# Optimization experiments

Measured on AMD Instinct MI355X. Metric: run time of the kernel, lower is better.

The kernel has to match this reference:

```python
import jax, jax.numpy as jnp
import numpy as np
import math

H = 16
D_MODEL = 1024
D_K = D_MODEL // H


def setup_inputs() -> dict:
    key = jax.random.key(0)
    ks = jax.random.split(key, 12)
    B, S = 4, 2048
    inp = {
        "query": jax.random.normal(ks[0], (B, S, D_MODEL), jnp.float32),
        "key": jax.random.normal(ks[1], (B, S, D_MODEL), jnp.float32),
        "value": jax.random.normal(ks[2], (B, S, D_MODEL), jnp.float32),
        # causal mask, broadcastable over heads: [B, 1, S, S]
        "mask": jnp.broadcast_to(jnp.tril(jnp.ones((S, S), bool)), (B, 1, S, S)),
    }
    sc = 1.0 / math.sqrt(D_MODEL)
    inp["Wq"] = jax.random.normal(ks[3], (D_MODEL, D_MODEL), jnp.float32) * sc
    inp["bq"] = jnp.zeros((D_MODEL,), jnp.float32)
    inp["Wk"] = jax.random.normal(ks[4], (D_MODEL, D_MODEL), jnp.float32) * sc
    inp["bk"] = jnp.zeros((D_MODEL,), jnp.float32)
    inp["Wv"] = jax.random.normal(ks[5], (D_MODEL, D_MODEL), jnp.float32) * sc
    inp["bv"] = jnp.zeros((D_MODEL,), jnp.float32)
    inp["Wo"] = jax.random.normal(ks[6], (D_MODEL, D_MODEL), jnp.float32) * sc
    inp["bo"] = jnp.zeros((D_MODEL,), jnp.float32)
    return inp


def reference(query, key, value, mask, Wq, bq, Wk, bk, Wv, bv, Wo, bo):
    B, S, D = query.shape
    # torch nn.Linear: y = x @ W.T + b; then view(B,-1,h,d_k).transpose(1,2)
    def proj(x, W, b):
        return (x @ W.T + b).reshape(B, -1, H, D_K).transpose(0, 2, 1, 3)  # [B,h,S,d_k]

    q = proj(query, Wq, bq)
    k = proj(key, Wk, bk)
    v = proj(value, Wv, bv)

    scores = jnp.einsum("bhqd,bhkd->bhqk", q, k) / math.sqrt(D_K)
    scores = jnp.where(mask, scores, jnp.finfo(scores.dtype).min)
    p_attn = jax.nn.softmax(scores, axis=-1)  # dropout: eval mode (identity)
    x = jnp.einsum("bhqk,bhkd->bhqd", p_attn, v)
    x = x.transpose(0, 2, 1, 3).reshape(B, -1, H * D_K)
    return x @ Wo.T + bo
```

## Files before the change

kernel.cpp:

```cpp
#include <hip/hip_runtime.h>
#include <hip/hip_bf16.h>

typedef unsigned short u16;
typedef unsigned int u32;
typedef __attribute__((ext_vector_type(8))) short short8;
typedef __attribute__((ext_vector_type(4))) short short4v;
typedef __attribute__((ext_vector_type(4))) float f32x4;
typedef __attribute__((ext_vector_type(4))) float float4_t;

#define DIM 1024
#define NH  16
#define DKK 64
#define SEQ 2048
#define NB  4
#define HDSZ ((size_t)NB * NH * SEQ * DKK)
#define WSZ  ((size_t)DIM * DIM)
#define SM_SCALE 0.1803368801111244f

__device__ __forceinline__ u16 f2bf(float f) {
    __bf16 h = (__bf16)f;
    return __builtin_bit_cast(u16, h);
}

__device__ __forceinline__ f32x4 mfma_bf16(short8 a, short8 b, f32x4 c) {
    return __builtin_amdgcn_mfma_f32_16x16x32_bf16(a, b, c, 0, 0, 0);
}

__device__ __forceinline__ short8 pack8(float4_t a, float4_t b) {
    short8 v;
    v[0] = (short)f2bf(a[0]); v[1] = (short)f2bf(a[1]);
    v[2] = (short)f2bf(a[2]); v[3] = (short)f2bf(a[3]);
    v[4] = (short)f2bf(b[0]); v[5] = (short)f2bf(b[1]);
    v[6] = (short)f2bf(b[2]); v[7] = (short)f2bf(b[3]);
    return v;
}

typedef const __attribute__((address_space(1))) u32* gas1_t;
typedef __attribute__((address_space(3))) u32* las3_t;
__device__ __forceinline__ void g2l16(const void* g, void* l) {
    __builtin_amdgcn_global_load_lds((gas1_t)g, (las3_t)l, 16, 0, 0);
}

__device__ __forceinline__ float max16(const f32x4* s) {
    const float a = fmaxf(fmaxf(s[0][0], s[0][1]), fmaxf(s[0][2], s[0][3]));
    const float b = fmaxf(fmaxf(s[1][0], s[1][1]), fmaxf(s[1][2], s[1][3]));
    const float c = fmaxf(fmaxf(s[2][0], s[2][1]), fmaxf(s[2][2], s[2][3]));
    const float d = fmaxf(fmaxf(s[3][0], s[3][1]), fmaxf(s[3][2], s[3][3]));
    return fmaxf(fmaxf(a, b), fmaxf(c, d));
}

__global__ __launch_bounds__(256)
void convall(const float* __restrict__ q, const float* __restrict__ k,
             const float* __restrict__ v,
             const float* __restrict__ w0, const float* __restrict__ w1,
             const float* __restrict__ w2, const float* __restrict__ w3,
             u16* __restrict__ dq, u16* __restrict__ dk, u16* __restrict__ dv,
             u16* __restrict__ dw)
{
    const int y = blockIdx.y;
    const float* src;
    u16* dst;
    if (y < 4) {
        src = y == 0 ? w0 : y == 1 ? w1 : y == 2 ? w2 : w3;
        dst = dw + (size_t)y * WSZ;
    } else {
        const int a = (y - 4) >> 3, c = (y - 4) & 7;
        src = (a == 0 ? q : a == 1 ? k : v) + (size_t)c * WSZ;
        dst = (a == 0 ? dq : a == 1 ? dk : dv) + (size_t)c * WSZ;
    }
    const size_t i = ((size_t)blockIdx.x * 256 + threadIdx.x) * 8;
    const float4_t a = *(const float4_t*)(src + i);
    const float4_t b = *(const float4_t*)(src + i + 4);
    *(short8*)(dst + i) = pack8(a, b);
}

template<int MODE>
__global__ __launch_bounds__(256)
void gemmb(const u16* __restrict__ A0, const u16* __restrict__ A1,
           const u16* __restrict__ Wb,
           const float* __restrict__ b0, const float* __restrict__ b1,
           u16* __restrict__ Cb, float* __restrict__ Cf)
{
    __shared__ __align__(16) u16 As[128][64];
    __shared__ __align__(16) u16 Bs[128][64];
    const int tid  = threadIdx.x;
    const int lane = tid & 63;
    const int w    = tid >> 6;
    const int wr   = w >> 1, wc = w & 1;
    const int m0   = blockIdx.y * 128;
    const int n0   = blockIdx.x * 128;
    const int z    = (MODE == 0) ? blockIdx.z : 0;
    const int lm   = lane & 15, lg = lane >> 4;
    const int srow   = lane >> 3;
    const int schunk = (lane & 7) ^ srow;

    const u16* A  = (MODE == 0) ? (z ? A1 : A0) : A0;
    const u16* Bw = (MODE == 2) ? A1 : Wb + (size_t)z * WSZ;

    f32x4 acc[4][4];
#pragma unroll
    for (int i = 0; i < 4; ++i)
#pragma unroll
        for (int j = 0; j < 4; ++j) acc[i][j] = (f32x4){0.f, 0.f, 0.f, 0.f};

    for (int k0 = 0; k0 < DIM; k0 += 64) {
        __syncthreads();
#pragma unroll
        for (int i = 0; i < 4; ++i) {
            g2l16(A  + (size_t)(m0 + w * 32 + i * 8 + srow) * DIM + k0 + schunk * 8,
                  &As[w * 32 + i * 8][0]);
            g2l16(Bw + (size_t)(n0 + w * 32 + i * 8 + srow) * DIM + k0 + schunk * 8,
                  &Bs[w * 32 + i * 8][0]);
        }
        __syncthreads();

        short8 af[2][4], bfr[2][4];
#pragma unroll
        for (int t = 0; t < 4; ++t)
#pragma unroll
            for (int kh = 0; kh < 2; ++kh) {
                const int c = (kh * 4 + lg) ^ (lm & 7);
                af[kh][t]  = *(const short8*)&As[wr * 64 + t * 16 + lm][c * 8];
                bfr[kh][t] = *(const short8*)&Bs[wc * 64 + t * 16 + lm][c * 8];
            }
#pragma unroll
        for (int mt = 0; mt < 4; ++mt)
#pragma unroll
            for (int nt = 0; nt < 4; ++nt) {
                acc[mt][nt] = mfma_bf16(af[0][mt], bfr[0][nt], acc[mt][nt]);
                acc[mt][nt] = mfma_bf16(af[1][mt], bfr[1][nt], acc[mt][nt]);
            }
    }

    const float scale = (MODE == 0 && z == 0) ? SM_SCALE : 1.f;
    const float* bias = (MODE == 0 && z) ? b1 : b0;
    u16* Cz = (MODE == 0) ? Cb + (size_t)z * HDSZ : Cb;

#pragma unroll
    for (int mt = 0; mt < 4; ++mt)
#pragma unroll
        for (int nt = 0; nt < 4; ++nt)
#pragma unroll
            for (int r = 0; r < 4; ++r) {
                const int m = m0 + wr * 64 + mt * 16 + lg * 4 + r;
                const int n = n0 + wc * 64 + nt * 16 + lm;
                if (MODE == 0) {
                    const float val = (acc[mt][nt][r] + bias[n]) * scale;
                    const int b = m >> 11, s = m & 2047;
                    const int h = n >> 6,  dk = n & 63;
                    Cz[(((size_t)b * NH + h) * SEQ + s) * DKK + dk] = f2bf(val);
                } else if (MODE == 1) {
                    Cf[(size_t)m * DIM + n] = acc[mt][nt][r] + bias[n];
                } else {
                    const float val = acc[mt][nt][r] + bias[m];
                    const int h = m >> 6, dk = m & 63;
                    const int b = n >> 11, s = n & 2047;
                    Cz[(((size_t)b * NH + h) * DKK + dk) * SEQ + s] = f2bf(val);
                }
            }
}

__global__ __launch_bounds__(256, 2)
void attn3(const u16* __restrict__ Q, const u16* __restrict__ K,
           const u16* __restrict__ Vt, u16* __restrict__ O)
{
    __shared__ __align__(16) u16 Ks[64][72];
    __shared__ __align__(16) u16 Vs[64][72];
    __shared__ __align__(16) u16 Ps[4][32][72];

    const int tid  = threadIdx.x;
    const int lane = tid & 63;
    const int w    = tid >> 6;
    const int lm   = lane & 15, lg = lane >> 4;
    const int Lr   = blockIdx.y * gridDim.x + blockIdx.x;
    const int work = (Lr & 7) * 128 + (Lr >> 3);
    const int pb   = work & 15;
    const int bh   = work >> 4;
    const int Abase = pb * 64;
    const int Bbase = SEQ - 64 - Abase;
    const int qA = Abase + 16 * w;
    const int qB = Bbase + 16 * w;
    const u16* Qp = Q  + (size_t)bh * SEQ * DKK;
    const u16* Kp = K  + (size_t)bh * SEQ * DKK;
    const u16* Vp = Vt + (size_t)bh * DKK * SEQ;

    short8 qa[2][2];
#pragma unroll
    for (int kh = 0; kh < 2; ++kh) {
        qa[0][kh] = *(const short8*)(Qp + (size_t)(qA + lm) * DKK + kh * 32 + lg * 8);
        qa[1][kh] = *(const short8*)(Qp + (size_t)(qB + lm) * DKK + kh * 32 + lg * 8);
    }

    float m_q[2] = {-INFINITY, -INFINITY};
    float l_q[2] = {0.f, 0.f};
    f32x4 o[2][4];
#pragma unroll
    for (int qt = 0; qt < 2; ++qt)
#pragma unroll
        for (int dt = 0; dt < 4; ++dt) o[qt][dt] = (f32x4){0.f, 0.f, 0.f, 0.f};

    const f32x4 zero = (f32x4){0.f, 0.f, 0.f, 0.f};
    const int srow = tid >> 3;
    const int soct = (tid & 7) * 8;
    const int kv_end = Bbase + 64;

    short8 rk0 = *(const short8*)(Kp + (size_t)srow * DKK + soct);
    short8 rk1 = *(const short8*)(Kp + (size_t)(srow + 32) * DKK + soct);
    short8 rv0 = *(const short8*)(Vp + (size_t)srow * SEQ + soct);
    short8 rv1 = *(const short8*)(Vp + (size_t)(srow + 32) * SEQ + soct);

    for (int kv0 = 0; kv0 < kv_end; kv0 += 64) {
        __syncthreads();
        *(short8*)&Ks[srow][soct]      = rk0;
        *(short8*)&Ks[srow + 32][soct] = rk1;
        *(short8*)&Vs[srow][soct]      = rv0;
        *(short8*)&Vs[srow + 32][soct] = rv1;
        const int nkv = kv0 + 64;
        if (nkv < kv_end) {
            rk0 = *(const short8*)(Kp + (size_t)(nkv + srow) * DKK + soct);
            rk1 = *(const short8*)(Kp + (size_t)(nkv + srow + 32) * DKK + soct);
            rv0 = *(const short8*)(Vp + (size_t)srow * SEQ + nkv + soct);
            rv1 = *(const short8*)(Vp + (size_t)(srow + 32) * SEQ + nkv + soct);
        }
        __syncthreads();

        const bool actA = kv0 < qA + 16;
        const bool msk[2] = { kv0 + 63 > qA, kv0 + 63 > qB };
        const int  qb[2]  = { qA, qB };

        f32x4 s[2][4];
#pragma unroll
        for (int kvt = 0; kvt < 4; ++kvt) {
            const short8 kb0 = *(const short8*)&Ks[kvt * 16 + lm][lg * 8];
            const short8 kb1 = *(const short8*)&Ks[kvt * 16 + lm][32 + lg * 8];
            s[1][kvt] = mfma_bf16(kb1, qa[1][1], mfma_bf16(kb0, qa[1][0], zero));
            if (actA)
                s[0][kvt] = mfma_bf16(kb1, qa[0][1], mfma_bf16(kb0, qa[0][0], zero));
        }

        float mx[2] = {-INFINITY, -INFINITY};
#pragma unroll
        for (int qt = 0; qt < 2; ++qt) {
            if (!qt && !actA) continue;
            if (msk[qt]) {
                const int q = qb[qt] + lm;
#pragma unroll
                for (int kvt = 0; kvt < 4; ++kvt)
#pragma unroll
                    for (int r = 0; r < 4; ++r) {
                        const int kv = kv0 + kvt * 16 + lg * 4 + r;
                        if (kv > q) s[qt][kvt][r] = -INFINITY;
                    }
            }
            float vmax = max16(s[qt]);
            vmax = fmaxf(vmax, __shfl_xor(vmax, 16));
            vmax = fmaxf(vmax, __shfl_xor(vmax, 32));
            mx[qt] = vmax;
        }

        const bool small = (!actA || mx[0] <= m_q[0] + 8.f) && (mx[1] <= m_q[1] + 8.f);
        if (__all(small)) {
#pragma unroll
            for (int qt = 0; qt < 2; ++qt) {
                if (!qt && !actA) continue;
                float part[4];
#pragma unroll
                for (int kvt = 0; kvt < 4; ++kvt) {
                    short4v pk;
                    f32x4 p;
#pragma unroll
                    for (int r = 0; r < 4; ++r) {
                        p[r] = __builtin_exp2f(s[qt][kvt][r] - m_q[qt]);
                        pk[r] = (short)f2bf(p[r]);
                    }
                    part[kvt] = (p[0] + p[1]) + (p[2] + p[3]);
                    *(short4v*)&Ps[w][qt * 16 + lm][kvt * 16 + lg * 4] = pk;
                }
                l_q[qt] += (part[0] + part[1]) + (part[2] + part[3]);
            }
        } else {
#pragma unroll
            for (int qt = 0; qt < 2; ++qt) {
                if (!qt && !actA) continue;
                const float mnew = fmaxf(m_q[qt], mx[qt]);
                const float alpha = __builtin_exp2f(m_q[qt] - mnew);
                m_q[qt] = mnew;
                float part[4];
#pragma unroll
                for (int kvt = 0; kvt < 4; ++kvt) {
                    short4v pk;
                    f32x4 p;
#pragma unroll
                    for (int r = 0; r < 4; ++r) {
                        p[r] = __builtin_exp2f(s[qt][kvt][r] - mnew);
                        pk[r] = (short)f2bf(p[r]);
                    }
                    part[kvt] = (p[0] + p[1]) + (p[2] + p[3]);
                    *(short4v*)&Ps[w][qt * 16 + lm][kvt * 16 + lg * 4] = pk;
                }
                l_q[qt] = l_q[qt] * alpha + (part[0] + part[1]) + (part[2] + part[3]);
#pragma unroll
                for (int r = 0; r < 4; ++r) {
                    const float ar = __shfl(alpha, lg * 4 + r);
#pragma unroll
                    for (int dt = 0; dt < 4; ++dt) o[qt][dt][r] *= ar;
                }
            }
        }
        asm volatile("s_waitcnt lgkmcnt(0)" ::: "memory");

        short8 pa[2][2], vbt[4][2];
#pragma unroll
        for (int qt = 0; qt < 2; ++qt)
            if (qt || actA) {
                pa[qt][0] = *(const short8*)&Ps[w][qt * 16 + lm][lg * 8];
                pa[qt][1] = *(const short8*)&Ps[w][qt * 16 + lm][32 + lg * 8];
            }
#pragma unroll
        for (int dt = 0; dt < 4; ++dt) {
            vbt[dt][0] = *(const short8*)&Vs[dt * 16 + lm][lg * 8];
            vbt[dt][1] = *(const short8*)&Vs[dt * 16 + lm][32 + lg * 8];
        }
#pragma unroll
        for (int dt = 0; dt < 4; ++dt)
#pragma unroll
            for (int qt = 0; qt < 2; ++qt) {
                if (!qt && !actA) continue;
                o[qt][dt] = mfma_bf16(pa[qt][1], vbt[dt][1],
                                      mfma_bf16(pa[qt][0], vbt[dt][0], o[qt][dt]));
            }
    }

    const int b = bh >> 4, h = bh & 15;
#pragma unroll
    for (int qt = 0; qt < 2; ++qt) {
        float lf = l_q[qt];
        lf += __shfl_xor(lf, 16);
        lf += __shfl_xor(lf, 32);
        const int qbase = qt ? qB : qA;
#pragma unroll
        for (int r = 0; r < 4; ++r) {
            const float li = 1.f / __shfl(lf, lg * 4 + r);
            const int srw = qbase + lg * 4 + r;
#pragma unroll
            for (int dt = 0; dt < 4; ++dt)
                O[(((size_t)b * SEQ + srw) * NH + h) * DKK + dt * 16 + lm] =
                    f2bf(o[qt][dt][r] * li);
        }
    }
}

extern "C" void kernel_launch(void* const* d_in, const int* in_sizes, int n_in,
                              void* d_out, int out_size, void* d_ws, size_t ws_size,
                              hipStream_t stream)
{
    const float* query = (const float*)d_in[0];
    const float* key   = (const float*)d_in[1];
    const float* value = (const float*)d_in[2];
    const float* Wq = (const float*)d_in[4];
    const float* bq = (const float*)d_in[5];
    const float* Wk = (const float*)d_in[6];
    const float* bk = (const float*)d_in[7];
    const float* Wv = (const float*)d_in[8];
    const float* bv = (const float*)d_in[9];
    const float* Wo = (const float*)d_in[10];
    const float* bo = (const float*)d_in[11];
    float* out = (float*)d_out;

    u16* qws  = (u16*)d_ws;
    u16* kws  = qws + HDSZ;
    u16* vtws = kws + HDSZ;
    u16* ows  = vtws + HDSZ;
    u16* wbf  = ows + HDSZ;
    u16* vbf  = wbf + 4 * WSZ;

    dim3 gqk(DIM / 128, (NB * SEQ) / 128, 2);
    dim3 gv((NB * SEQ) / 128, DIM / 128);
    dim3 gg(DIM / 128, (NB * SEQ) / 128);

    convall<<<dim3(WSZ / 2048, 28), 256, 0, stream>>>(
        query, key, value, Wq, Wk, Wv, Wo, ows, vtws, vbf, wbf);
    gemmb<0><<<gqk, 256, 0, stream>>>(ows, vtws, wbf, bq, bk, qws, nullptr);
    gemmb<2><<<gv, 256, 0, stream>>>(wbf + 2 * WSZ, vbf, nullptr, bv, nullptr,
                                     vtws, nullptr);
    attn3<<<dim3(16, NB * NH), 256, 0, stream>>>(qws, kws, vtws, ows);
    gemmb<1><<<gg, 256, 0, stream>>>(ows, nullptr, wbf + 3 * WSZ, bo, nullptr,
                                     nullptr, out);
}
```

Measured before the change: 228.4 us.

## Rewrite attention kernel with 32x32 MFMA and register-resident P operand

Replaces the 16x16x32 MFMA attention kernel with one using 32x32x16 bf16 MFMA. Each wave now owns 32 query rows, either in the near or the far tile of the balanced pair, instead of 16 rows from each. The softmax probabilities are rearranged across lanes with shuffles and fed straight into the PV MFMA, so the per-wave P shared-memory buffer and its round trip are gone. The change also drops the occupancy hint of 2 blocks per CU and uses a small shared buffer to broadcast the rescale and normalisation factors. The risks are higher register pressure from the 16-wide accumulators and a possible load imbalance between waves on the short and long causal halves.

```diff
diff --git a/kernel.cpp b/kernel.cpp
--- a/kernel.cpp
+++ b/kernel.cpp
@@ -6,7 +6,9 @@
 typedef __attribute__((ext_vector_type(8))) short short8;
 typedef __attribute__((ext_vector_type(4))) short short4v;
 typedef __attribute__((ext_vector_type(4))) float f32x4;
+typedef __attribute__((ext_vector_type(16))) float f32x16;
 typedef __attribute__((ext_vector_type(4))) float float4_t;
+typedef __attribute__((ext_vector_type(4))) u32 u32x4;
 
 #define DIM 1024
 #define NH  16
@@ -26,6 +28,10 @@
     return __builtin_amdgcn_mfma_f32_16x16x32_bf16(a, b, c, 0, 0, 0);
 }
 
+__device__ __forceinline__ f32x16 mfma32(short8 a, short8 b, f32x16 c) {
+    return __builtin_amdgcn_mfma_f32_32x32x16_bf16(a, b, c, 0, 0, 0);
+}
+
 __device__ __forceinline__ short8 pack8(float4_t a, float4_t b) {
     short8 v;
     v[0] = (short)f2bf(a[0]); v[1] = (short)f2bf(a[1]);
@@ -41,11 +47,11 @@
     __builtin_amdgcn_global_load_lds((gas1_t)g, (las3_t)l, 16, 0, 0);
 }
 
-__device__ __forceinline__ float max16(const f32x4* s) {
-    const float a = fmaxf(fmaxf(s[0][0], s[0][1]), fmaxf(s[0][2], s[0][3]));
-    const float b = fmaxf(fmaxf(s[1][0], s[1][1]), fmaxf(s[1][2], s[1][3]));
-    const float c = fmaxf(fmaxf(s[2][0], s[2][1]), fmaxf(s[2][2], s[2][3]));
-    const float d = fmaxf(fmaxf(s[3][0], s[3][1]), fmaxf(s[3][2], s[3][3]));
+__device__ __forceinline__ float tree16(const f32x16& v) {
+    const float a = fmaxf(fmaxf(v[0], v[1]),  fmaxf(v[2], v[3]));
+    const float b = fmaxf(fmaxf(v[4], v[5]),  fmaxf(v[6], v[7]));
+    const float c = fmaxf(fmaxf(v[8], v[9]),  fmaxf(v[10], v[11]));
+    const float d = fmaxf(fmaxf(v[12], v[13]), fmaxf(v[14], v[15]));
     return fmaxf(fmaxf(a, b), fmaxf(c, d));
 }
 
@@ -160,46 +166,40 @@
             }
 }
 
-__global__ __launch_bounds__(256, 2)
-void attn3(const u16* __restrict__ Q, const u16* __restrict__ K,
+__global__ __launch_bounds__(256)
+void attn6(const u16* __restrict__ Q, const u16* __restrict__ K,
            const u16* __restrict__ Vt, u16* __restrict__ O)
 {
     __shared__ __align__(16) u16 Ks[64][72];
     __shared__ __align__(16) u16 Vs[64][72];
-    __shared__ __align__(16) u16 Ps[4][32][72];
+    __shared__ float Bx[4][32];
 
     const int tid  = threadIdx.x;
     const int lane = tid & 63;
     const int w    = tid >> 6;
-    const int lm   = lane & 15, lg = lane >> 4;
+    const int l31  = lane & 31;
+    const int h    = lane >> 5;
     const int Lr   = blockIdx.y * gridDim.x + blockIdx.x;
     const int work = (Lr & 7) * 128 + (Lr >> 3);
     const int pb   = work & 15;
     const int bh   = work >> 4;
     const int Abase = pb * 64;
     const int Bbase = SEQ - 64 - Abase;
-    const int qA = Abase + 16 * w;
-    const int qB = Bbase + 16 * w;
+    const int qbase = (w < 2) ? (Abase + 32 * w) : (Bbase + 32 * (w - 2));
     const u16* Qp = Q  + (size_t)bh * SEQ * DKK;
     const u16* Kp = K  + (size_t)bh * SEQ * DKK;
     const u16* Vp = Vt + (size_t)bh * DKK * SEQ;
 
-    short8 qa[2][2];
-#pragma unroll
-    for (int kh = 0; kh < 2; ++kh) {
-        qa[0][kh] = *(const short8*)(Qp + (size_t)(qA + lm) * DKK + kh * 32 + lg * 8);
-        qa[1][kh] = *(const short8*)(Qp + (size_t)(qB + lm) * DKK + kh * 32 + lg * 8);
-    }
-
-    float m_q[2] = {-INFINITY, -INFINITY};
-    float l_q[2] = {0.f, 0.f};
-    f32x4 o[2][4];
-#pragma unroll
-    for (int qt = 0; qt < 2; ++qt)
-#pragma unroll
-        for (int dt = 0; dt < 4; ++dt) o[qt][dt] = (f32x4){0.f, 0.f, 0.f, 0.f};
-
-    const f32x4 zero = (f32x4){0.f, 0.f, 0.f, 0.f};
+    short8 qa[4];
+#pragma unroll
+    for (int ks = 0; ks < 4; ++ks)
+        qa[ks] = *(const short8*)(Qp + (size_t)(qbase + l31) * DKK + ks * 16 + h * 8);
+
+    float m_q = -INFINITY, l_q = 0.f;
+    f32x16 o0, o1;
+#pragma unroll
+    for (int r = 0; r < 16; ++r) { o0[r] = 0.f; o1[r] = 0.f; }
+
     const int srow = tid >> 3;
     const int soct = (tid & 7) * 8;
     const int kv_end = Bbase + 64;
@@ -224,129 +224,130 @@
         }
         __syncthreads();
 
-        const bool actA = kv0 < qA + 16;
-        const bool msk[2] = { kv0 + 63 > qA, kv0 + 63 > qB };
-        const int  qb[2]  = { qA, qB };
-
-        f32x4 s[2][4];
-#pragma unroll
-        for (int kvt = 0; kvt < 4; ++kvt) {
-            const short8 kb0 = *(const short8*)&Ks[kvt * 16 + lm][lg * 8];
-            const short8 kb1 = *(const short8*)&Ks[kvt * 16 + lm][32 + lg * 8];
-            s[1][kvt] = mfma_bf16(kb1, qa[1][1], mfma_bf16(kb0, qa[1][0], zero));
-            if (actA)
-                s[0][kvt] = mfma_bf16(kb1, qa[0][1], mfma_bf16(kb0, qa[0][0], zero));
+        const bool act = kv0 < qbase + 32;
+        if (act) {
+            const bool act1 = kv0 < qbase;
+            const bool msk  = kv0 + 63 > qbase;
+
+            f32x16 s0, s1;
+#pragma unroll
+            for (int r = 0; r < 16; ++r) s0[r] = 0.f;
+#pragma unroll
+            for (int ks = 0; ks < 4; ++ks)
+                s0 = mfma32(*(const short8*)&Ks[l31][ks * 16 + h * 8], qa[ks], s0);
+            if (act1) {
+#pragma unroll
+                for (int r = 0; r < 16; ++r) s1[r] = 0.f;
+#pragma unroll
+                for (int ks = 0; ks < 4; ++ks)
+                    s1 = mfma32(*(const short8*)&Ks[32 + l31][ks * 16 + h * 8], qa[ks], s1);
+            }
+
+            if (msk) {
+                const int qg = qbase + l31;
+#pragma unroll
+                for (int r = 0; r < 16; ++r) {
+                    const int kvg = kv0 + (r & 3) + 8 * (r >> 2) + 4 * h;
+                    if (kvg > qg) s0[r] = -INFINITY;
+                }
+                if (act1) {
+#pragma unroll
+                    for (int r = 0; r < 16; ++r) {
+                        const int kvg = kv0 + 32 + (r & 3) + 8 * (r >> 2) + 4 * h;
+                        if (kvg > qg) s1[r] = -INFINITY;
+                    }
+                }
+            }
+
+            float mx = tree16(s0);
+            if (act1) mx = fmaxf(mx, tree16(s1));
+            mx = fmaxf(mx, __shfl_xor(mx, 32));
+
+            float mc = m_q;
+            if (!__all(mx <= m_q + 8.f)) {
+                mc = fmaxf(m_q, mx);
+                const float alpha = __builtin_exp2f(m_q - mc);
+                m_q = mc;
+                Bx[w][l31] = alpha;
+                asm volatile("s_waitcnt lgkmcnt(0)" ::: "memory");
+#pragma unroll
+                for (int r = 0; r < 16; ++r) {
+                    const float ar = Bx[w][(r & 3) + 8 * (r >> 2) + 4 * h];
+                    o0[r] *= ar; o1[r] *= ar;
+                }
+                l_q *= alpha;
+            }
+
+            u32 wd[8], wq[8];
+            {
+                float ps = 0.f;
+#pragma unroll
+                for (int m8 = 0; m8 < 8; ++m8) {
+                    const float p0 = __builtin_exp2f(s0[2 * m8] - mc);
+                    const float p1 = __builtin_exp2f(s0[2 * m8 + 1] - mc);
+                    ps += p0 + p1;
+                    wd[m8] = (u32)f2bf(p0) | ((u32)f2bf(p1) << 16);
+                }
+                l_q += ps;
+#pragma unroll
+                for (int m8 = 0; m8 < 8; ++m8)
+                    wq[m8] = (u32)__shfl_xor((int)wd[m8], 32);
+#pragma unroll
+                for (int ks = 0; ks < 2; ++ks) {
+                    const int base = ks * 4;
+                    u32x4 aw;
+                    aw[0] = h ? wq[base + 2] : wd[base];
+                    aw[1] = h ? wq[base + 3] : wd[base + 1];
+                    aw[2] = h ? wd[base + 2] : wq[base];
+                    aw[3] = h ? wd[base + 3] : wq[base + 1];
+                    const short8 af = __builtin_bit_cast(short8, aw);
+                    const int col = ks * 16 + h * 8;
+                    o0 = mfma32(af, *(const short8*)&Vs[l31][col], o0);
+                    o1 = mfma32(af, *(const short8*)&Vs[32 + l31][col], o1);
+                }
+            }
+            if (act1) {
+                float ps = 0.f;
+#pragma unroll
+                for (int m8 = 0; m8 < 8; ++m8) {
+                    const float p0 = __builtin_exp2f(s1[2 * m8] - mc);
+                    const float p1 = __builtin_exp2f(s1[2 * m8 + 1] - mc);
+                    ps += p0 + p1;
+                    wd[m8] = (u32)f2bf(p0) | ((u32)f2bf(p1) << 16);
+                }
+                l_q += ps;
+#pragma unroll
+                for (int m8 = 0; m8 < 8; ++m8)
+                    wq[m8] = (u32)__shfl_xor((int)wd[m8], 32);
+#pragma unroll
+                for (int ks = 0; ks < 2; ++ks) {
+                    const int base = ks * 4;
+                    u32x4 aw;
+                    aw[0] = h ? wq[base + 2] : wd[base];
+                    aw[1] = h ? wq[base + 3] : wd[base + 1];
+                    aw[2] = h ? wd[base + 2] : wq[base];
+                    aw[3] = h ? wd[base + 3] : wq[base + 1];
+                    const short8 af = __builtin_bit_cast(short8, aw);
+                    const int col = 32 + ks * 16 + h * 8;
+                    o0 = mfma32(af, *(const short8*)&Vs[l31][col], o0);
+                    o1 = mfma32(af, *(const short8*)&Vs[32 + l31][col], o1);
+                }
+            }
         }
-
-        float mx[2] = {-INFINITY, -INFINITY};
-#pragma unroll
-        for (int qt = 0; qt < 2; ++qt) {
-            if (!qt && !actA) continue;
-            if (msk[qt]) {
-                const int q = qb[qt] + lm;
-#pragma unroll
-                for (int kvt = 0; kvt < 4; ++kvt)
-#pragma unroll
-                    for (int r = 0; r < 4; ++r) {
-                        const int kv = kv0 + kvt * 16 + lg * 4 + r;
-                        if (kv > q) s[qt][kvt][r] = -INFINITY;
-                    }
-            }
-            float vmax = max16(s[qt]);
-            vmax = fmaxf(vmax, __shfl_xor(vmax, 16));
-            vmax = fmaxf(vmax, __shfl_xor(vmax, 32));
-            mx[qt] = vmax;
-        }
-
-        const bool small = (!actA || mx[0] <= m_q[0] + 8.f) && (mx[1] <= m_q[1] + 8.f);
-        if (__all(small)) {
-#pragma unroll
-            for (int qt = 0; qt < 2; ++qt) {
-                if (!qt && !actA) continue;
-                float part[4];
-#pragma unroll
-                for (int kvt = 0; kvt < 4; ++kvt) {
-                    short4v pk;
-                    f32x4 p;
-#pragma unroll
-                    for (int r = 0; r < 4; ++r) {
-                        p[r] = __builtin_exp2f(s[qt][kvt][r] - m_q[qt]);
-                        pk[r] = (short)f2bf(p[r]);
-                    }
-                    part[kvt] = (p[0] + p[1]) + (p[2] + p[3]);
-                    *(short4v*)&Ps[w][qt * 16 + lm][kvt * 16 + lg * 4] = pk;
-                }
-                l_q[qt] += (part[0] + part[1]) + (part[2] + part[3]);
-            }
-        } else {
-#pragma unroll
-            for (int qt = 0; qt < 2; ++qt) {
-                if (!qt && !actA) continue;
-                const float mnew = fmaxf(m_q[qt], mx[qt]);
-                const float alpha = __builtin_exp2f(m_q[qt] - mnew);
-                m_q[qt] = mnew;
-                float part[4];
-#pragma unroll
-                for (int kvt = 0; kvt < 4; ++kvt) {
-                    short4v pk;
-                    f32x4 p;
-#pragma unroll
-                    for (int r = 0; r < 4; ++r) {
-                        p[r] = __builtin_exp2f(s[qt][kvt][r] - mnew);
-                        pk[r] = (short)f2bf(p[r]);
-                    }
-                    part[kvt] = (p[0] + p[1]) + (p[2] + p[3]);
-                    *(short4v*)&Ps[w][qt * 16 + lm][kvt * 16 + lg * 4] = pk;
-                }
-                l_q[qt] = l_q[qt] * alpha + (part[0] + part[1]) + (part[2] + part[3]);
-#pragma unroll
-                for (int r = 0; r < 4; ++r) {
-                    const float ar = __shfl(alpha, lg * 4 + r);
-#pragma unroll
-                    for (int dt = 0; dt < 4; ++dt) o[qt][dt][r] *= ar;
-                }
-            }
-        }
-        asm volatile("s_waitcnt lgkmcnt(0)" ::: "memory");
-
-        short8 pa[2][2], vbt[4][2];
-#pragma unroll
-        for (int qt = 0; qt < 2; ++qt)
-            if (qt || actA) {
-                pa[qt][0] = *(const short8*)&Ps[w][qt * 16 + lm][lg * 8];
-                pa[qt][1] = *(const short8*)&Ps[w][qt * 16 + lm][32 + lg * 8];
-            }
-#pragma unroll
-        for (int dt = 0; dt < 4; ++dt) {
-            vbt[dt][0] = *(const short8*)&Vs[dt * 16 + lm][lg * 8];
-            vbt[dt][1] = *(const short8*)&Vs[dt * 16 + lm][32 + lg * 8];
-        }
-#pragma unroll
-        for (int dt = 0; dt < 4; ++dt)
-#pragma unroll
-            for (int qt = 0; qt < 2; ++qt) {
-                if (!qt && !actA) continue;
-                o[qt][dt] = mfma_bf16(pa[qt][1], vbt[dt][1],
-                                      mfma_bf16(pa[qt][0], vbt[dt][0], o[qt][dt]));
-            }
     }
 
-    const int b = bh >> 4, h = bh & 15;
-#pragma unroll
-    for (int qt = 0; qt < 2; ++qt) {
-        float lf = l_q[qt];
-        lf += __shfl_xor(lf, 16);
-        lf += __shfl_xor(lf, 32);
-        const int qbase = qt ? qB : qA;
-#pragma unroll
-        for (int r = 0; r < 4; ++r) {
-            const float li = 1.f / __shfl(lf, lg * 4 + r);
-            const int srw = qbase + lg * 4 + r;
-#pragma unroll
-            for (int dt = 0; dt < 4; ++dt)
-                O[(((size_t)b * SEQ + srw) * NH + h) * DKK + dt * 16 + lm] =
-                    f2bf(o[qt][dt][r] * li);
-        }
+    l_q += __shfl_xor(l_q, 32);
+    Bx[w][l31] = l_q;
+    asm volatile("s_waitcnt lgkmcnt(0)" ::: "memory");
+    const int b = bh >> 4, hh = bh & 15;
+#pragma unroll
+    for (int r = 0; r < 16; ++r) {
+        const int qlocal = (r & 3) + 8 * (r >> 2) + 4 * h;
+        const float li = 1.f / Bx[w][qlocal];
+        const int srw = qbase + qlocal;
+        u16* orow = O + (((size_t)b * SEQ + srw) * NH + hh) * DKK;
+        orow[l31]      = f2bf(o0[r] * li);
+        orow[32 + l31] = f2bf(o1[r] * li);
     }
 }
 
@@ -383,7 +384,7 @@
     gemmb<0><<<gqk, 256, 0, stream>>>(ows, vtws, wbf, bq, bk, qws, nullptr);
     gemmb<2><<<gv, 256, 0, stream>>>(wbf + 2 * WSZ, vbf, nullptr, bv, nullptr,
                                      vtws, nullptr);
-    attn3<<<dim3(16, NB * NH), 256, 0, stream>>>(qws, kws, vtws, ows);
+    attn6<<<dim3(16, NB * NH), 256, 0, stream>>>(qws, kws, vtws, ows);
     gemmb<1><<<gg, 256, 0, stream>>>(ows, nullptr, wbf + 3 * WSZ, bo, nullptr,
                                      nullptr, out);
 }
```

After: 265.5 us. 1.16x slower.
